# Kernel tuning notes

Measured on AMD Instinct MI355X. Metric: run time of the kernel, lower is better.

## Reference

```python
import jax, jax.numpy as jnp
import numpy as np

N = 20000      # points
K = 16         # neighbor pairs per query per branch
M = N * K      # total pairs
C = 384        # embed_dim
H = 6          # num_heads
HD = C // H    # head_dim = 64
H1 = H // 2    # cartesian-branch heads
L = 24         # quant_grid_length (window 6.0 / quant 0.25)
Q = 0.25       # quant_size
LS = 24        # quant_grid_length_sphere (120 / 5)
QS = 5.0       # quant_size_sphere
A = 0.05 * 0.25  # exponential_split 'a'
SCALE = HD ** -0.5


def setup_inputs() -> dict:
    key = jax.random.key(0)
    ks = jax.random.split(key, 12)
    s = 0.02
    inp = {}
    inp["query_feats"] = jax.random.normal(ks[0], (N, C), jnp.float32)
    inp["xyz"] = jax.random.uniform(ks[1], (N, 3), jnp.float32, -3.0, 3.0)
    inp["index_0"] = jnp.repeat(jnp.arange(N, dtype=jnp.int32), K)
    inp["index_1"] = jax.random.randint(ks[2], (M,), 0, N, dtype=jnp.int32)
    inp["index_0_sphere"] = jnp.repeat(jnp.arange(N, dtype=jnp.int32), K)
    inp["index_1_sphere"] = jax.random.randint(ks[3], (M,), 0, N, dtype=jnp.int32)
    inp["W_qkv"] = jax.random.normal(ks[4], (C, 3 * C), jnp.float32) * s
    inp["b_qkv"] = jnp.zeros((3 * C,), jnp.float32)
    inp["W_proj"] = jax.random.normal(ks[5], (C, C), jnp.float32) * s
    inp["b_proj"] = jnp.zeros((C,), jnp.float32)
    inp["tq"] = jax.random.normal(ks[6], (2 * L - 1, 3, H1, HD), jnp.float32) * s
    inp["tk"] = jax.random.normal(ks[7], (2 * L - 1, 3, H1, HD), jnp.float32) * s
    inp["tv"] = jax.random.normal(ks[8], (2 * L - 1, 3, H1, HD), jnp.float32) * s
    inp["tq_s"] = jax.random.normal(ks[9], (2 * LS, 3, H - H1, HD), jnp.float32) * s
    inp["tk_s"] = jax.random.normal(ks[10], (2 * LS, 3, H - H1, HD), jnp.float32) * s
    inp["tv_s"] = jax.random.normal(ks[11], (2 * LS, 3, H - H1, HD), jnp.float32) * s
    return inp


def _cart2sphere(xyz):
    x, y, z = xyz[:, 0], xyz[:, 1], xyz[:, 2]
    theta = (jnp.arctan2(y, x) + np.pi) * (180.0 / np.pi)
    beta = jnp.arctan2(jnp.sqrt(x * x + y * y), z) * (180.0 / np.pi)
    r = jnp.sqrt(x * x + y * y + z * z)
    return jnp.stack([theta, beta, r], -1)


def _rel_idx_cart(xyz, i0, i1):
    rel = xyz[i0] - xyz[i1]  # [M,3]
    idx = jnp.floor(rel / Q).astype(jnp.int32) + (L - 1)
    return jnp.clip(idx, 0, 2 * L - 2)


def _rel_idx_sphere(sph, i0, i1):
    rel = sph[i0] - sph[i1]  # [M,3] (theta, beta, r)
    idx01 = jnp.clip(jnp.floor(rel[:, :2] / QS).astype(jnp.int32) + LS, 0, 2 * LS - 1)
    # exponential_split on radial dim
    r = rel[:, 2]
    ra = jnp.abs(r)
    flag = (r >= 0).astype(jnp.float32)
    idx = 2.0 * jnp.floor(jnp.log((ra + 2.0 * A) / A) / np.log(2.0)) - 2.0
    idx = idx + ((3.0 * jnp.exp2(jnp.floor(idx / 2.0)) - 2.0) * A <= ra).astype(jnp.float32)
    idx = idx * (2.0 * flag - 1.0) + (flag - 1.0)
    idx2 = jnp.clip(idx.astype(jnp.int32) + 24, 0, 2 * LS - 1)
    return jnp.concatenate([idx01, idx2[:, None]], 1)


def _branch(q, k, v, i0, i1, rel_idx, Tq, Tk, Tv):
    # q,k,v: [N,h,d]; i0/i1: [M]; rel_idx: [M,3]; tables: [R,3,h,d]
    qg = q[i0]  # [M,h,d]
    kg = k[i1]
    attn = jnp.einsum('mhd,mhd->mh', qg, kg)
    for dim in range(3):
        attn = attn + jnp.einsum('mhd,mhd->mh', qg, Tq[rel_idx[:, dim], dim])
        attn = attn + jnp.einsum('mhd,mhd->mh', kg, Tk[rel_idx[:, dim], dim])
    # segment softmax over queries (i0)
    seg_max = jax.ops.segment_max(attn, i0, num_segments=N)
    ex = jnp.exp(attn - seg_max[i0])
    p = ex / jax.ops.segment_sum(ex, i0, num_segments=N)[i0]  # [M,h]
    vg = v[i1] + Tv[rel_idx[:, 0], 0] + Tv[rel_idx[:, 1], 1] + Tv[rel_idx[:, 2], 2]
    return jax.ops.segment_sum(p[:, :, None] * vg, i0, num_segments=N)  # [N,h,d]


def reference(query_feats, xyz, index_0, index_1, index_0_sphere, index_1_sphere,
              W_qkv, b_qkv, W_proj, b_proj, tq, tk, tv, tq_s, tk_s, tv_s):
    i0 = index_0.astype(jnp.int32)
    i1 = index_1.astype(jnp.int32)
    i0s = index_0_sphere.astype(jnp.int32)
    i1s = index_1_sphere.astype(jnp.int32)
    qkv = (query_feats @ W_qkv + b_qkv).reshape(N, 3, H, HD)
    q = qkv[:, 0] * SCALE
    k = qkv[:, 1]
    v = qkv[:, 2]
    sph = _cart2sphere(xyz)
    ri = _rel_idx_cart(xyz, i0, i1)
    out1 = _branch(q[:, :H1], k[:, :H1], v[:, :H1], i0, i1, ri, tq, tk, tv)
    ri_s = _rel_idx_sphere(sph, i0s, i1s)
    out2 = _branch(q[:, H1:], k[:, H1:], v[:, H1:], i0s, i1s, ri_s, tq_s, tk_s, tv_s)
    x = jnp.concatenate([out1, out2], 1).reshape(N, C)
    return x @ W_proj + b_proj
```

## Files before the change

kernel.cpp:

```cpp
#include <hip/hip_runtime.h>
#include <hip/hip_bf16.h>

namespace {

constexpr int NP   = 20000;
constexpr int CD   = 384;
constexpr int QKVD = 1152;
constexpr int TC   = 47 * 3 * 3 * 64;
constexpr int TS   = 48 * 3 * 3 * 64;

typedef __attribute__((ext_vector_type(8))) short short8;
typedef __attribute__((ext_vector_type(4))) float f32x4;
typedef __attribute__((ext_vector_type(2))) float f32x2;

__device__ inline float f32_atan2(float y, float x) {
  return (float)atan2((double)y, (double)x);
}
__device__ inline float f32_log(float x) {
  return (float)log((double)x);
}

__device__ inline float bfl(unsigned u) {
  union { unsigned u; float f; } c; c.u = u << 16; return c.f;
}
__device__ inline float bfh(unsigned u) {
  union { unsigned u; float f; } c; c.u = u & 0xffff0000u; return c.f;
}
__device__ inline f32x2 up2(unsigned u) {
  f32x2 r;
  r.x = bfl(u);
  r.y = bfh(u);
  return r;
}
__device__ inline unsigned short f2bf(float x) {
  __hip_bfloat16 hb = __float2bfloat16(x);
  unsigned short u; __builtin_memcpy(&u, &hb, 2);
  return u;
}

__device__ inline void async16(const void* g, void* l) {
  __builtin_amdgcn_global_load_lds(
      (const __attribute__((address_space(1))) unsigned int*)g,
      (__attribute__((address_space(3))) unsigned int*)l,
      16, 0, 0);
}

__global__ __launch_bounds__(256) void cvt_bf16_k(const float* __restrict__ in,
                                                  unsigned short* __restrict__ out, int n) {
  int i = (blockIdx.x * 256 + threadIdx.x) * 4;
  if (i < n) {
    float4 v = *(const float4*)(in + i);
    ushort4 o;
    o.x = f2bf(v.x); o.y = f2bf(v.y); o.z = f2bf(v.z); o.w = f2bf(v.w);
    *(ushort4*)(out + i) = o;
  }
}

__global__ __launch_bounds__(256) void transpose_cvt_k(const float* __restrict__ in,
                                                       unsigned short* __restrict__ out,
                                                       int R, int Cc) {
  __shared__ float t[32][33];
  int c0 = blockIdx.x * 32, r0 = blockIdx.y * 32;
  int tx = threadIdx.x, ty = threadIdx.y;
  #pragma unroll
  for (int i = 0; i < 32; i += 8)
    t[ty + i][tx] = in[(size_t)(r0 + ty + i) * Cc + (c0 + tx)];
  __syncthreads();
  #pragma unroll
  for (int i = 0; i < 32; i += 8)
    out[(size_t)(c0 + ty + i) * R + (r0 + tx)] = f2bf(t[tx][ty + i]);
}

__global__ __launch_bounds__(256) void prep_k(const float* __restrict__ tq,
                                              const float* __restrict__ tk,
                                              const float* __restrict__ tv,
                                              const float* __restrict__ tqs,
                                              const float* __restrict__ tks,
                                              const float* __restrict__ tvs,
                                              unsigned short* __restrict__ tq_b,
                                              unsigned short* __restrict__ tk_b,
                                              unsigned short* __restrict__ tv_b,
                                              unsigned short* __restrict__ tqs_b,
                                              unsigned short* __restrict__ tks_b,
                                              unsigned short* __restrict__ tvs_b,
                                              const float* __restrict__ xyz,
                                              float* __restrict__ sph) {
  const int y = blockIdx.y;
  const int t = blockIdx.x * 256 + threadIdx.x;
  if (y < 6) {
    const float* in = (y == 0) ? tq : (y == 1) ? tk : (y == 2) ? tv
                    : (y == 3) ? tqs : (y == 4) ? tks : tvs;
    unsigned short* out = (y == 0) ? tq_b : (y == 1) ? tk_b : (y == 2) ? tv_b
                        : (y == 3) ? tqs_b : (y == 4) ? tks_b : tvs_b;
    const int n = (y < 3) ? TC : TS;
    int i = t * 4;
    if (i < n) {
      float4 v = *(const float4*)(in + i);
      ushort4 o;
      o.x = f2bf(v.x); o.y = f2bf(v.y); o.z = f2bf(v.z); o.w = f2bf(v.w);
      *(ushort4*)(out + i) = o;
    }
  } else {
#pragma clang fp contract(off)
    #pragma unroll
    for (int r = 0; r < 4; ++r) {
      int i = t * 4 + r;
      if (i < NP) {
        const float PIF = 3.14159265358979323846f;
        const float R2D = 57.29577951308232f;
        float x = xyz[i * 3 + 0], yy = xyz[i * 3 + 1], z = xyz[i * 3 + 2];
        float sxy = x * x + yy * yy;
        sph[i * 3 + 0] = (f32_atan2(yy, x) + PIF) * R2D;
        sph[i * 3 + 1] = f32_atan2(sqrtf(sxy), z) * R2D;
        sph[i * 3 + 2] = sqrtf(sxy + z * z);
      }
    }
  }
}

template <int MODE>
__global__ __launch_bounds__(256) void gemm_async_k(const short* __restrict__ A,
                                                    const short* __restrict__ BT,
                                                    const float* __restrict__ bias,
                                                    void* __restrict__ Cout,
                                                    int M, int Nn, int K) {
  __shared__ short As[2][128][32];
  __shared__ short Bs[2][128][32];
  const int tid  = threadIdx.x;
  const int m0   = blockIdx.x * 128, n0 = blockIdx.y * 128;
  const int wave = tid >> 6, lane = tid & 63;
  const int wm   = (wave & 1) * 64, wn = (wave >> 1) * 64;
  const int quad = lane >> 4, l16 = lane & 15;
  const int srow = lane >> 2;
  const int scol = (lane & 3) * 8;

  f32x4 acc[4][4] = {};

  auto stage = [&](int buf, int k0) {
    #pragma unroll
    for (int c = 0; c < 2; ++c) {
      const int base = (wave + c * 4) * 16;
      const int gmr = m0 + base + srow;
      if (gmr < M)
        async16(A + (size_t)gmr * K + k0 + scol, &As[buf][base][0]);
      const int gnr = n0 + base + srow;
      if (gnr < Nn)
        async16(BT + (size_t)gnr * K + k0 + scol, &Bs[buf][base][0]);
    }
  };

  stage(0, 0);
  int cur = 0;
  for (int k0 = 0; k0 < K; k0 += 32) {
    __syncthreads();
    if (k0 + 32 < K) stage(cur ^ 1, k0 + 32);
    short8 af[4], bg[4];
    #pragma unroll
    for (int i = 0; i < 4; ++i) af[i] = *(const short8*)&As[cur][wm + i * 16 + l16][quad * 8];
    #pragma unroll
    for (int j = 0; j < 4; ++j) bg[j] = *(const short8*)&Bs[cur][wn + j * 16 + l16][quad * 8];
    #pragma unroll
    for (int i = 0; i < 4; ++i)
      #pragma unroll
      for (int j = 0; j < 4; ++j)
        acc[i][j] = __builtin_amdgcn_mfma_f32_16x16x32_bf16(af[i], bg[j], acc[i][j], 0, 0, 0);
    cur ^= 1;
  }

  #pragma unroll
  for (int i = 0; i < 4; ++i) {
    #pragma unroll
    for (int j = 0; j < 4; ++j) {
      int gn = n0 + wn + j * 16 + l16;
      if (gn >= Nn) continue;
      float bval = bias[gn];
      #pragma unroll
      for (int r = 0; r < 4; ++r) {
        int gm = m0 + wm + i * 16 + quad * 4 + r;
        if (gm < M) {
          float v = acc[i][j][r] + bval;
          if (MODE == 0) {
            if (gn < 384) v *= 0.125f;
            ((unsigned short*)Cout)[(size_t)gm * Nn + gn] = f2bf(v);
          } else {
            ((float*)Cout)[(size_t)gm * Nn + gn] = v;
          }
        }
      }
    }
  }
}

__device__ inline f32x2 dot8_pk(uint4 q, uint4 k, uint4 a0, uint4 a1, uint4 a2,
                                uint4 t0, uint4 t1, uint4 t2, f32x2 acc) {
  const unsigned* qp = &q.x;  const unsigned* kp = &k.x;
  const unsigned* a0p = &a0.x; const unsigned* a1p = &a1.x; const unsigned* a2p = &a2.x;
  const unsigned* t0p = &t0.x; const unsigned* t1p = &t1.x; const unsigned* t2p = &t2.x;
  #pragma unroll
  for (int w2 = 0; w2 < 4; ++w2) {
    f32x2 qf = up2(qp[w2]), kf = up2(kp[w2]);
    f32x2 tqs = up2(a0p[w2]) + up2(a1p[w2]) + up2(a2p[w2]);
    f32x2 tks = up2(t0p[w2]) + up2(t1p[w2]) + up2(t2p[w2]);
    acc += qf * (kf + tqs) + kf * tks;
  }
  return acc;
}

__global__ __launch_bounds__(256) void attn3_k(const unsigned short* __restrict__ qkv,
                                               const float* __restrict__ xyz,
                                               const float* __restrict__ sph,
                                               const int* __restrict__ nb_c,
                                               const int* __restrict__ nb_s,
                                               const unsigned short* __restrict__ tq_c,
                                               const unsigned short* __restrict__ tk_c,
                                               const unsigned short* __restrict__ tv_c,
                                               const unsigned short* __restrict__ tq_s,
                                               const unsigned short* __restrict__ tk_s,
                                               const unsigned short* __restrict__ tv_s,
                                               unsigned short* __restrict__ xout) {
  __shared__ int   s_i1 [4][16];
  __shared__ int   s_off[4][16][3];
  __shared__ float s_attn[4][3][16];
  __shared__ float s_p   [4][3][16];

  const int w    = threadIdx.x >> 6;
  const int lane = threadIdx.x & 63;
  const int n    = blockIdx.x * 2 + (w >> 1);
  const int b    = w & 1;

  const unsigned short* tqb = b ? tq_s : tq_c;
  const unsigned short* tkb = b ? tk_s : tk_c;
  const unsigned short* tvb = b ? tv_s : tv_c;

  if (lane < 16) {
#pragma clang fp contract(off)
    const int e = lane;
    if (b == 0) {
      const int i1 = nb_c[n * 16 + e];
      s_i1[w][e] = i1;
      const float rel[3] = {xyz[n * 3 + 0] - xyz[i1 * 3 + 0],
                            xyz[n * 3 + 1] - xyz[i1 * 3 + 1],
                            xyz[n * 3 + 2] - xyz[i1 * 3 + 2]};
      #pragma unroll
      for (int dim = 0; dim < 3; ++dim) {
        int idx = (int)floorf(rel[dim] * 4.0f) + 23;
        idx = min(max(idx, 0), 46);
        s_off[w][e][dim] = (idx * 3 + dim) * 192;
      }
    } else {
      const int i1 = nb_s[n * 16 + e];
      s_i1[w][e] = i1;
      const float d0 = sph[n * 3 + 0] - sph[i1 * 3 + 0];
      const float d1 = sph[n * 3 + 1] - sph[i1 * 3 + 1];
      const float dr = sph[n * 3 + 2] - sph[i1 * 3 + 2];
      int i0a = (int)floorf(d0 / 5.0f) + 24;
      int i1a = (int)floorf(d1 / 5.0f) + 24;
      const float ra = fabsf(dr);
      const float flag = (dr >= 0.0f) ? 1.0f : 0.0f;
      const float t = (ra + 0.025f) / 0.0125f;
      const float wv = f32_log(t) / 0.69314718055994531f;
      float fidx = 2.0f * floorf(wv) - 2.0f;
      fidx += ((3.0f * exp2f(floorf(fidx * 0.5f)) - 2.0f) * 0.0125f <= ra) ? 1.0f : 0.0f;
      fidx = fidx * (2.0f * flag - 1.0f) + (flag - 1.0f);
      int i2a = (int)fidx + 24;
      s_off[w][e][0] = (min(max(i0a, 0), 47) * 3 + 0) * 192;
      s_off[w][e][1] = (min(max(i1a, 0), 47) * 3 + 1) * 192;
      s_off[w][e][2] = (min(max(i2a, 0), 47) * 3 + 2) * 192;
    }
  }

  const int eg = lane >> 2, g = lane & 3;
  const int goff = g * 16;
  {
    const int i1 = s_i1[w][eg];
    const int o0 = s_off[w][eg][0];
    const int o1 = s_off[w][eg][1];
    const int o2 = s_off[w][eg][2];
    const unsigned short* kp = qkv + (size_t)i1 * QKVD + 384 + b * 192 + goff;
    const unsigned short* qp = qkv + (size_t)n * QKVD + b * 192 + goff;
    #pragma unroll
    for (int hh = 0; hh < 3; ++hh) {
      const int ho = hh * 64;
      uint4 kv0 = *(const uint4*)(kp + ho);
      uint4 kv1 = *(const uint4*)(kp + ho + 8);
      uint4 qv0 = *(const uint4*)(qp + ho);
      uint4 qv1 = *(const uint4*)(qp + ho + 8);
      uint4 a00 = *(const uint4*)(tqb + o0 + ho + goff);
      uint4 a01 = *(const uint4*)(tqb + o0 + ho + goff + 8);
      uint4 a10 = *(const uint4*)(tqb + o1 + ho + goff);
      uint4 a11 = *(const uint4*)(tqb + o1 + ho + goff + 8);
      uint4 a20 = *(const uint4*)(tqb + o2 + ho + goff);
      uint4 a21 = *(const uint4*)(tqb + o2 + ho + goff + 8);
      uint4 b00 = *(const uint4*)(tkb + o0 + ho + goff);
      uint4 b01 = *(const uint4*)(tkb + o0 + ho + goff + 8);
      uint4 b10 = *(const uint4*)(tkb + o1 + ho + goff);
      uint4 b11 = *(const uint4*)(tkb + o1 + ho + goff + 8);
      uint4 b20 = *(const uint4*)(tkb + o2 + ho + goff);
      uint4 b21 = *(const uint4*)(tkb + o2 + ho + goff + 8);
      f32x2 acc2 = {0.0f, 0.0f};
      acc2 = dot8_pk(qv0, kv0, a00, a10, a20, b00, b10, b20, acc2);
      acc2 = dot8_pk(qv1, kv1, a01, a11, a21, b01, b11, b21, acc2);
      float acc = acc2.x + acc2.y;
      acc += __shfl_xor(acc, 1);
      acc += __shfl_xor(acc, 2);
      if (g == 0) s_attn[w][hh][eg] = acc;
    }
  }

  if (lane < 48) {
    const int hh = lane >> 4, ee = lane & 15;
    float a = s_attn[w][hh][ee];
    float m = a;
    #pragma unroll
    for (int off = 8; off > 0; off >>= 1) m = fmaxf(m, __shfl_xor(m, off));
    float ex = __expf(a - m);
    float s = ex;
    #pragma unroll
    for (int off = 8; off > 0; off >>= 1) s += __shfl_xor(s, off);
    s_p[w][hh][ee] = ex / s;
  }

  {
    const int half = lane >> 5;
    const int dl   = lane & 31;
    f32x2 vacc[3] = {{0.0f, 0.0f}, {0.0f, 0.0f}, {0.0f, 0.0f}};
    #pragma unroll
    for (int ep = 0; ep < 8; ++ep) {
      const int e2 = ep * 2 + half;
      const int j1 = s_i1[w][e2];
      const int p0 = s_off[w][e2][0];
      const int p1 = s_off[w][e2][1];
      const int p2 = s_off[w][e2][2];
      const unsigned short* vp = qkv + (size_t)j1 * QKVD + 768 + b * 192 + dl * 2;
      #pragma unroll
      for (int hh = 0; hh < 3; ++hh) {
        const int ho = hh * 64;
        const unsigned vv = *(const unsigned*)(vp + ho);
        const unsigned t0 = *(const unsigned*)(tvb + p0 + ho + dl * 2);
        const unsigned t1 = *(const unsigned*)(tvb + p1 + ho + dl * 2);
        const unsigned t2 = *(const unsigned*)(tvb + p2 + ho + dl * 2);
        const float pr = s_p[w][hh][e2];
        f32x2 prv = {pr, pr};
        f32x2 sum = up2(vv) + up2(t0) + up2(t1) + up2(t2);
        vacc[hh] += prv * sum;
      }
    }
    #pragma unroll
    for (int hh = 0; hh < 3; ++hh) {
      vacc[hh].x += __shfl_xor(vacc[hh].x, 32);
      vacc[hh].y += __shfl_xor(vacc[hh].y, 32);
    }
    if (lane < 32) {
      #pragma unroll
      for (int hh = 0; hh < 3; ++hh) {
        unsigned o = ((unsigned)f2bf(vacc[hh].y) << 16) | (unsigned)f2bf(vacc[hh].x);
        *(unsigned*)(xout + (size_t)n * CD + (b * 3 + hh) * 64 + dl * 2) = o;
      }
    }
  }
}

}

extern "C" void kernel_launch(void* const* d_in, const int* in_sizes, int n_in,
                              void* d_out, int out_size, void* d_ws, size_t ws_size,
                              hipStream_t stream) {
  const float* qf    = (const float*)d_in[0];
  const float* xyz   = (const float*)d_in[1];
  const int*   i1c   = (const int*)d_in[3];
  const int*   i1s   = (const int*)d_in[5];
  const float* Wqkv  = (const float*)d_in[6];
  const float* bqkv  = (const float*)d_in[7];
  const float* Wproj = (const float*)d_in[8];
  const float* bproj = (const float*)d_in[9];
  const float* tq    = (const float*)d_in[10];
  const float* tk    = (const float*)d_in[11];
  const float* tv    = (const float*)d_in[12];
  const float* tqs   = (const float*)d_in[13];
  const float* tks   = (const float*)d_in[14];
  const float* tvs   = (const float*)d_in[15];

  char* w = (char*)d_ws;
  unsigned short* qf_b   = (unsigned short*)w; w += (size_t)NP * CD * 2;
  unsigned short* wqkvT  = (unsigned short*)w; w += (size_t)QKVD * CD * 2;
  unsigned short* wprojT = (unsigned short*)w; w += (size_t)CD * CD * 2;
  unsigned short* qkv_b  = (unsigned short*)w; w += (size_t)NP * QKVD * 2;
  unsigned short* x_b    = (unsigned short*)w; w += (size_t)NP * CD * 2;
  float*          sph    = (float*)w;          w += (size_t)NP * 3 * 4;
  unsigned short* tq_b   = (unsigned short*)w; w += (size_t)TC * 2;
  unsigned short* tk_b   = (unsigned short*)w; w += (size_t)TC * 2;
  unsigned short* tv_b   = (unsigned short*)w; w += (size_t)TC * 2;
  unsigned short* tqs_b  = (unsigned short*)w; w += (size_t)TS * 2;
  unsigned short* tks_b  = (unsigned short*)w; w += (size_t)TS * 2;
  unsigned short* tvs_b  = (unsigned short*)w;

  cvt_bf16_k<<<(NP * CD / 4 + 255) / 256, 256, 0, stream>>>(qf, qf_b, NP * CD);
  transpose_cvt_k<<<dim3(QKVD / 32, CD / 32), dim3(32, 8), 0, stream>>>(Wqkv, wqkvT, CD, QKVD);
  transpose_cvt_k<<<dim3(CD / 32, CD / 32), dim3(32, 8), 0, stream>>>(Wproj, wprojT, CD, CD);
  prep_k<<<dim3(27, 7), 256, 0, stream>>>(tq, tk, tv, tqs, tks, tvs,
                                          tq_b, tk_b, tv_b, tqs_b, tks_b, tvs_b, xyz, sph);

  gemm_async_k<0><<<dim3((NP + 127) / 128, QKVD / 128), 256, 0, stream>>>(
      (const short*)qf_b, (const short*)wqkvT, bqkv, qkv_b, NP, QKVD, CD);

  attn3_k<<<NP / 2, 256, 0, stream>>>(qkv_b, xyz, sph, i1c, i1s,
                                      tq_b, tk_b, tv_b, tqs_b, tks_b, tvs_b, x_b);

  gemm_async_k<1><<<dim3((NP + 127) / 128, CD / 128), 256, 0, stream>>>(
      (const short*)x_b, (const short*)wprojT, bproj, d_out, NP, CD, CD);
}
```

Before: 323.4 us.

## Use bf16 dot2 for QK scores and vectorize V aggregation with 16-byte loads

The score computation now uses the hardware bf16 fdot2 instruction (when the builtin exists) instead of unpacking bf16 to float and doing packed FMAs. The value-aggregation phase is remapped so each lane handles 8 channels of one neighbor with uint4 loads rather than 2 channels with 4-byte loads. The partial sums are then reduced across neighbors with xor shuffles and written with 16-byte stores. This cuts instruction count and load count per wave, at the cost of more shuffle reductions and slightly different rounding from the bf16 dot.

Result: faster. 310.3 us (-4.1%).

```diff
diff --git a/kernel.cpp b/kernel.cpp
--- a/kernel.cpp
+++ b/kernel.cpp
@@ -37,6 +37,17 @@
   unsigned short u; __builtin_memcpy(&u, &hb, 2);
   return u;
 }
+
+#if __has_builtin(__builtin_amdgcn_fdot2_f32_bf16)
+#define HAVE_BF16_DOT 1
+typedef __attribute__((ext_vector_type(2))) __bf16 bf16x2_t;
+__device__ inline float dot2bf(unsigned a, unsigned b, float c) {
+  bf16x2_t av, bv;
+  __builtin_memcpy(&av, &a, 4);
+  __builtin_memcpy(&bv, &b, 4);
+  return __builtin_amdgcn_fdot2_f32_bf16(av, bv, c, false);
+}
+#endif
 
 __device__ inline void async16(const void* g, void* l) {
   __builtin_amdgcn_global_load_lds(
@@ -206,6 +217,15 @@
   return acc;
 }
 
+__device__ inline void acc4(f32x2* vc, uint4 vv, uint4 t0, uint4 t1, uint4 t2,
+                            float pr) {
+  f32x2 prv = {pr, pr};
+  vc[0] += prv * (up2(vv.x) + up2(t0.x) + up2(t1.x) + up2(t2.x));
+  vc[1] += prv * (up2(vv.y) + up2(t0.y) + up2(t1.y) + up2(t2.y));
+  vc[2] += prv * (up2(vv.z) + up2(t0.z) + up2(t1.z) + up2(t2.z));
+  vc[3] += prv * (up2(vv.w) + up2(t0.w) + up2(t1.w) + up2(t2.w));
+}
+
 __global__ __launch_bounds__(256) void attn3_k(const unsigned short* __restrict__ qkv,
                                                const float* __restrict__ xyz,
                                                const float* __restrict__ sph,
@@ -297,10 +317,31 @@
       uint4 b11 = *(const uint4*)(tkb + o1 + ho + goff + 8);
       uint4 b20 = *(const uint4*)(tkb + o2 + ho + goff);
       uint4 b21 = *(const uint4*)(tkb + o2 + ho + goff + 8);
+      float acc;
+#ifdef HAVE_BF16_DOT
+      float aqk = 0.0f, aq0 = 0.0f, aq1 = 0.0f, aq2 = 0.0f;
+      float ak0 = 0.0f, ak1 = 0.0f, ak2 = 0.0f;
+#define DOT7(qd, kd, a0d, a1d, a2d, b0d, b1d, b2d)                         \
+      aqk = dot2bf(qd, kd, aqk);  aq0 = dot2bf(qd, a0d, aq0);              \
+      aq1 = dot2bf(qd, a1d, aq1); aq2 = dot2bf(qd, a2d, aq2);              \
+      ak0 = dot2bf(kd, b0d, ak0); ak1 = dot2bf(kd, b1d, ak1);              \
+      ak2 = dot2bf(kd, b2d, ak2);
+      DOT7(qv0.x, kv0.x, a00.x, a10.x, a20.x, b00.x, b10.x, b20.x)
+      DOT7(qv0.y, kv0.y, a00.y, a10.y, a20.y, b00.y, b10.y, b20.y)
+      DOT7(qv0.z, kv0.z, a00.z, a10.z, a20.z, b00.z, b10.z, b20.z)
+      DOT7(qv0.w, kv0.w, a00.w, a10.w, a20.w, b00.w, b10.w, b20.w)
+      DOT7(qv1.x, kv1.x, a01.x, a11.x, a21.x, b01.x, b11.x, b21.x)
+      DOT7(qv1.y, kv1.y, a01.y, a11.y, a21.y, b01.y, b11.y, b21.y)
+      DOT7(qv1.z, kv1.z, a01.z, a11.z, a21.z, b01.z, b11.z, b21.z)
+      DOT7(qv1.w, kv1.w, a01.w, a11.w, a21.w, b01.w, b11.w, b21.w)
+#undef DOT7
+      acc = ((aqk + aq0) + (aq1 + aq2)) + ((ak0 + ak1) + ak2);
+#else
       f32x2 acc2 = {0.0f, 0.0f};
       acc2 = dot8_pk(qv0, kv0, a00, a10, a20, b00, b10, b20, acc2);
       acc2 = dot8_pk(qv1, kv1, a01, a11, a21, b01, b11, b21, acc2);
-      float acc = acc2.x + acc2.y;
+      acc = acc2.x + acc2.y;
+#endif
       acc += __shfl_xor(acc, 1);
       acc += __shfl_xor(acc, 2);
       if (g == 0) s_attn[w][hh][eg] = acc;
@@ -321,40 +362,49 @@
   }
 
   {
-    const int half = lane >> 5;
-    const int dl   = lane & 31;
-    f32x2 vacc[3] = {{0.0f, 0.0f}, {0.0f, 0.0f}, {0.0f, 0.0f}};
-    #pragma unroll
-    for (int ep = 0; ep < 8; ++ep) {
-      const int e2 = ep * 2 + half;
-      const int j1 = s_i1[w][e2];
-      const int p0 = s_off[w][e2][0];
-      const int p1 = s_off[w][e2][1];
-      const int p2 = s_off[w][e2][2];
-      const unsigned short* vp = qkv + (size_t)j1 * QKVD + 768 + b * 192 + dl * 2;
+    const int e8 = lane >> 3;
+    const int c  = lane & 7;
+    const int offVa = s_i1[w][e8]     * QKVD + 768 + b * 192 + c * 8;
+    const int offVb = s_i1[w][e8 + 8] * QKVD + 768 + b * 192 + c * 8;
+    const int offA0 = s_off[w][e8][0] + c * 8;
+    const int offA1 = s_off[w][e8][1] + c * 8;
+    const int offA2 = s_off[w][e8][2] + c * 8;
+    const int offB0 = s_off[w][e8 + 8][0] + c * 8;
+    const int offB1 = s_off[w][e8 + 8][1] + c * 8;
+    const int offB2 = s_off[w][e8 + 8][2] + c * 8;
+    #pragma unroll
+    for (int hh = 0; hh < 3; ++hh) {
+      const int ho = hh * 64;
+      f32x2 vc[4] = {{0.f, 0.f}, {0.f, 0.f}, {0.f, 0.f}, {0.f, 0.f}};
+      {
+        uint4 vv = *(const uint4*)(qkv + offVa + ho);
+        uint4 t0 = *(const uint4*)(tvb + offA0 + ho);
+        uint4 t1 = *(const uint4*)(tvb + offA1 + ho);
+        uint4 t2 = *(const uint4*)(tvb + offA2 + ho);
+        acc4(vc, vv, t0, t1, t2, s_p[w][hh][e8]);
+      }
+      {
+        uint4 vv = *(const uint4*)(qkv + offVb + ho);
+        uint4 t0 = *(const uint4*)(tvb + offB0 + ho);
+        uint4 t1 = *(const uint4*)(tvb + offB1 + ho);
+        uint4 t2 = *(const uint4*)(tvb + offB2 + ho);
+        acc4(vc, vv, t0, t1, t2, s_p[w][hh][e8 + 8]);
+      }
       #pragma unroll
-      for (int hh = 0; hh < 3; ++hh) {
-        const int ho = hh * 64;
-        const unsigned vv = *(const unsigned*)(vp + ho);
-        const unsigned t0 = *(const unsigned*)(tvb + p0 + ho + dl * 2);
-        const unsigned t1 = *(const unsigned*)(tvb + p1 + ho + dl * 2);
-        const unsigned t2 = *(const unsigned*)(tvb + p2 + ho + dl * 2);
-        const float pr = s_p[w][hh][e2];
-        f32x2 prv = {pr, pr};
-        f32x2 sum = up2(vv) + up2(t0) + up2(t1) + up2(t2);
-        vacc[hh] += prv * sum;
-      }
-    }
-    #pragma unroll
-    for (int hh = 0; hh < 3; ++hh) {
-      vacc[hh].x += __shfl_xor(vacc[hh].x, 32);
-      vacc[hh].y += __shfl_xor(vacc[hh].y, 32);
-    }
-    if (lane < 32) {
-      #pragma unroll
-      for (int hh = 0; hh < 3; ++hh) {
-        unsigned o = ((unsigned)f2bf(vacc[hh].y) << 16) | (unsigned)f2bf(vacc[hh].x);
-        *(unsigned*)(xout + (size_t)n * CD + (b * 3 + hh) * 64 + dl * 2) = o;
+      for (int q4 = 0; q4 < 4; ++q4) {
+        #pragma unroll
+        for (int off = 8; off <= 32; off <<= 1) {
+          vc[q4].x += __shfl_xor(vc[q4].x, off);
+          vc[q4].y += __shfl_xor(vc[q4].y, off);
+        }
+      }
+      if (e8 == 0) {
+        uint4 o;
+        o.x = ((unsigned)f2bf(vc[0].y) << 16) | (unsigned)f2bf(vc[0].x);
+        o.y = ((unsigned)f2bf(vc[1].y) << 16) | (unsigned)f2bf(vc[1].x);
+        o.z = ((unsigned)f2bf(vc[2].y) << 16) | (unsigned)f2bf(vc[2].x);
+        o.w = ((unsigned)f2bf(vc[3].y) << 16) | (unsigned)f2bf(vc[3].x);
+        *(uint4*)(xout + (size_t)n * CD + (b * 3 + hh) * 64 + c * 8) = o;
       }
     }
   }
```
